# Kernel optimization log

Hardware: AMD Instinct MI355X
Metric: run time of the kernel (lower is better)

## Reference

```python
import jax, jax.numpy as jnp
import numpy as np

B, S, D = 2, 2048, 2048
H, DH = 16, 128  # heads, dhead


def setup_inputs() -> dict:
    key = jax.random.key(0)
    k1, k2, k3 = jax.random.split(key, 3)
    x = jax.random.normal(k1, (B, S, D), dtype=jnp.float32)
    # torch Linear weights: [out_features, in_features], fan_in-scaled init
    w_in = jax.random.normal(k2, (3 * H * DH, D), dtype=jnp.float32) * (1.0 / np.sqrt(D))
    w_out = jax.random.normal(k3, (D, H * DH), dtype=jnp.float32) * (1.0 / np.sqrt(H * DH))
    return {"x": x, "w_in": w_in, "w_out": w_out}


def reference(x, w_in, w_out):
    b, s, _ = x.shape
    # input projection (no bias): [b, s, 3*H*DH]
    projected = jnp.einsum("bsd,ed->bse", x, w_in)
    # view(b, s, H, 3*DH) then chunk along last dim -> q, k, v each [b, s, H, DH]
    projected = projected.reshape(b, s, H, 3 * DH)
    q, k, v = jnp.split(projected, 3, axis=-1)
    # naive path: scores [b, H, s, s]
    scores = jnp.einsum("bqhd,bkhd->bhqk", q, k) * (1.0 / np.sqrt(DH))
    # causal mask (tril keeps, upper triangle -> -inf)
    causal_mask = jnp.tril(jnp.ones((s, s), dtype=bool))
    scores = jnp.where(causal_mask, scores, jnp.float32(-jnp.inf))
    attn = jax.nn.softmax(scores, axis=-1)
    # PV: [b, s, H, DH]
    out = jnp.einsum("bhqk,bkhd->bqhd", attn, v)
    out = out.reshape(b, s, H * DH)
    # output projection (no bias): [b, s, D]
    return jnp.einsum("bse,de->bsd", out, w_out)
```

## Files before the change

kernel.cpp:

```cpp
#include <hip/hip_runtime.h>
#include <hip/hip_bf16.h>
#include <math.h>


typedef short bf16x8 __attribute__((ext_vector_type(8)));
typedef float f32x4 __attribute__((ext_vector_type(4)));

#define NEG_BIG -30000.0f

__device__ __forceinline__ short f2bf(float f) {
    union { float f; unsigned u; } v; v.f = f;
    unsigned r = v.u + 0x7fffu + ((v.u >> 16) & 1u);
    return (short)(r >> 16);
}

__device__ __forceinline__ int pack2bf(float a, float b) {
    return (int)((((unsigned)f2bf(b)) << 16) | (((unsigned)f2bf(a)) & 0xffffu));
}

#define GLDS16(g, l) \
    __builtin_amdgcn_global_load_lds((const __attribute__((address_space(1))) void*)(g), \
                                     (__attribute__((address_space(3))) void*)(l), 16, 0, 0)

__global__ __launch_bounds__(256) void cvt3_f32_bf16(const float* __restrict__ x,  short* __restrict__ dx,
                                                     const float* __restrict__ wi, short* __restrict__ dwi,
                                                     const float* __restrict__ wo, short* __restrict__ dwo,
                                                     int c1, int c2) {
    const int g = blockIdx.x * blockDim.x + threadIdx.x;
    const float* s; short* d; int off;
    if (g < c1)      { s = x;  d = dx;  off = g; }
    else if (g < c2) { s = wi; d = dwi; off = g - c1; }
    else             { s = wo; d = dwo; off = g - c2; }
    float4 v = *(const float4*)(s + (size_t)off * 4);
    short4 o;
    o.x = f2bf(v.x); o.y = f2bf(v.y); o.z = f2bf(v.z); o.w = f2bf(v.w);
    *(short4*)(d + (size_t)off * 4) = o;
}

template <int BN, bool F32OUT>
__global__ __launch_bounds__(256) void gemm_bt(const short* __restrict__ A,
                                               const short* __restrict__ Bm,
                                               void* __restrict__ Cv,
                                               int N, int K) {
    constexpr int NT = BN / 32;
    constexpr int SUBA = 128 * 32;
    constexpr int SUBB = BN * 32;
    __shared__ short sA[2 * SUBA];
    __shared__ short sB[2 * SUBB];
    const int lane = threadIdx.x & 63;
    const int w = threadIdx.x >> 6;
    const int l15 = lane & 15, quad = lane >> 4;
    const int bm0 = blockIdx.y * 128, bn0 = blockIdx.x * BN;

    const int c1 = w * 64 + lane;
    const short* gA = A + (size_t)(bm0 + (c1 >> 2)) * K + (c1 & 3) * 8;
    const short* gB = Bm + (size_t)(bn0 + (c1 >> 2)) * K + (c1 & 3) * 8;
    const size_t half64 = (size_t)64 * K;
    short* lA1 = sA + w * 512;
    short* lA2 = sA + 2048 + w * 512;
    short* lB1 = sB + w * 512;
    short* lB2 = sB + 2048 + w * 512;

    const int wm = (w >> 1) * 64, wn = (w & 1) * (BN / 2);
    const short* pa = sA + (wm + l15) * 32 + quad * 8;
    const short* pb = sB + (wn + l15) * 32 + quad * 8;

    f32x4 acc[4][NT] = {};
    for (int k0 = 0; k0 < K; k0 += 64) {
        #pragma unroll
        for (int s = 0; s < 2; s++) {
            const int ks = k0 + s * 32;
            GLDS16(gA + ks, lA1 + s * SUBA);
            GLDS16(gA + half64 + ks, lA2 + s * SUBA);
            GLDS16(gB + ks, lB1 + s * SUBB);
            if constexpr (BN == 128) GLDS16(gB + half64 + ks, lB2 + s * SUBB);
        }
        __syncthreads();
        #pragma unroll
        for (int s = 0; s < 2; s++) {
            bf16x8 af[4], bf[NT];
            #pragma unroll
            for (int mt = 0; mt < 4; mt++) af[mt] = *(const bf16x8*)(pa + s * SUBA + mt * 512);
            #pragma unroll
            for (int nt = 0; nt < NT; nt++) bf[nt] = *(const bf16x8*)(pb + s * SUBB + nt * 512);
            #pragma unroll
            for (int mt = 0; mt < 4; mt++)
                #pragma unroll
                for (int nt = 0; nt < NT; nt++)
                    acc[mt][nt] = __builtin_amdgcn_mfma_f32_16x16x32_bf16(af[mt], bf[nt], acc[mt][nt], 0, 0, 0);
        }
        __syncthreads();
    }
    #pragma unroll
    for (int mt = 0; mt < 4; mt++)
        #pragma unroll
        for (int nt = 0; nt < NT; nt++)
            #pragma unroll
            for (int r = 0; r < 4; r++) {
                int row = bm0 + wm + mt * 16 + quad * 4 + r;
                int col = bn0 + wn + nt * 16 + l15;
                if (F32OUT)
                    ((float*)Cv)[(size_t)row * N + col] = acc[mt][nt][r];
                else
                    ((short*)Cv)[(size_t)row * N + col] = f2bf(acc[mt][nt][r]);
            }
}

#define VP2 72
__global__ __launch_bounds__(512) void attn_kernel(const short* __restrict__ P,
                                                   short* __restrict__ O) {
    constexpr int S = 2048, ROWW = 6144, HD = 2048;
    const int id = blockIdx.x;
    const int b = id >> 8;
    const int rr = id & 255;
    const int h = rr & 15;
    const int t0 = rr >> 4;
    const int qt = b ? (15 - t0) : t0;
    const int wave = threadIdx.x >> 6, lane = threadIdx.x & 63;
    const int l15 = lane & 15, quad = lane >> 4;
    const int qRow = qt * 128 + wave * 16;
    const short* Pb = P + (size_t)b * S * ROWW;
    const short* Qp = Pb + h * 384;
    const short* Kp = Qp + 128;
    const short* Vp = Qp + 256;

    __shared__ short sK[2][64 * 128];
    __shared__ short sVt[2][128 * VP2];

    bf16x8 qf[4];
    #pragma unroll
    for (int f = 0; f < 4; f++)
        qf[f] = *(const bf16x8*)(Qp + (size_t)(qRow + l15) * ROWW + f * 32 + quad * 8);

    const bool isK = wave < 4;
    const int c1 = (wave & 3) * 64 + lane;
    const int krow1 = c1 >> 4;
    const int kcol = ((c1 & 15) ^ (krow1 & 15)) * 8;
    const short* gK1 = Kp + (size_t)krow1 * ROWW + kcol;
    const short* gK2 = Kp + (size_t)(krow1 + 16) * ROWW + kcol;
    const short* gK3 = Kp + (size_t)(krow1 + 32) * ROWW + kcol;
    const short* gK4 = Kp + (size_t)(krow1 + 48) * ROWW + kcol;
    const int ldsOff1 = (wave & 3) * 512;
    const int ldsOff2 = 2048 + ldsOff1;
    const int ldsOff3 = 4096 + ldsOff1;
    const int ldsOff4 = 6144 + ldsOff1;
    const int vt = (int)threadIdx.x - 256;
    const int vKey = vt & 31;
    const int vD0 = (vt >> 5) * 8;
    const short* gV = Vp + (size_t)vKey * ROWW + vD0;
    const short* gV2 = Vp + (size_t)(vKey + 32) * ROWW + vD0;

    const int kTiles = qt * 2 + 2;
    const float c2 = 0.12752741594977435f;
    const float THRR = 90.50966799f;
    const int qG = qRow + l15;

    f32x4 accO[8] = {};
    float m_i = NEG_BIG, l_i = 0.f;

    if (isK) {
        GLDS16(gK1, &sK[0][ldsOff1]);
        GLDS16(gK2, &sK[0][ldsOff2]);
        GLDS16(gK3, &sK[0][ldsOff3]);
        GLDS16(gK4, &sK[0][ldsOff4]);
    } else {
        bf16x8 v0 = *(const bf16x8*)(gV);
        bf16x8 v1 = *(const bf16x8*)(gV + 64);
        bf16x8 v2 = *(const bf16x8*)(gV2);
        bf16x8 v3 = *(const bf16x8*)(gV2 + 64);
        #pragma unroll
        for (int j = 0; j < 8; j++) {
            sVt[0][(vD0 + j) * VP2 + vKey] = v0[j];
            sVt[0][(vD0 + 64 + j) * VP2 + vKey] = v1[j];
            sVt[0][(vD0 + j) * VP2 + vKey + 32] = v2[j];
            sVt[0][(vD0 + 64 + j) * VP2 + vKey + 32] = v3[j];
        }
    }
    __syncthreads();

    for (int kt = 0; kt < kTiles; kt++) {
        const int cur = kt & 1, nxt = cur ^ 1;
        const bool pre = (kt + 1 < kTiles);
        bf16x8 v0n, v1n, v2n, v3n;
        if (pre) {
            const size_t kOff = (size_t)(kt + 1) * 64 * ROWW;
            if (isK) {
                GLDS16(gK1 + kOff, &sK[nxt][ldsOff1]);
                GLDS16(gK2 + kOff, &sK[nxt][ldsOff2]);
                GLDS16(gK3 + kOff, &sK[nxt][ldsOff3]);
                GLDS16(gK4 + kOff, &sK[nxt][ldsOff4]);
            } else {
                v0n = *(const bf16x8*)(gV + kOff);
                v1n = *(const bf16x8*)(gV + kOff + 64);
                v2n = *(const bf16x8*)(gV2 + kOff);
                v3n = *(const bf16x8*)(gV2 + kOff + 64);
            }
        }
        if (kt * 64 <= qRow + 15) {
            f32x4 sc[4] = {};
            #pragma unroll
            for (int f = 0; f < 4; f++) {
                const int jj = ((4 * f + quad) ^ l15) * 8;
                #pragma unroll
                for (int hh = 0; hh < 4; hh++) {
                    bf16x8 kf = *(const bf16x8*)(&sK[cur][(hh * 16 + l15) * 128 + jj]);
                    sc[hh] = __builtin_amdgcn_mfma_f32_16x16x32_bf16(kf, qf[f], sc[hh], 0, 0, 0);
                }
            }
            if (kt * 64 + 63 > qRow) {
                #pragma unroll
                for (int hh = 0; hh < 4; hh++)
                    #pragma unroll
                    for (int r = 0; r < 4; r++) {
                        const int key = kt * 64 + hh * 16 + quad * 4 + r;
                        if (key > qG) sc[hh][r] = NEG_BIG;
                    }
            }
            float mloc = sc[0][0];
            #pragma unroll
            for (int hh = 0; hh < 4; hh++)
                #pragma unroll
                for (int r = 0; r < 4; r++) mloc = fmaxf(mloc, sc[hh][r]);
            mloc = fmaxf(mloc, __shfl_xor(mloc, 16));
            mloc = fmaxf(mloc, __shfl_xor(mloc, 32));
            if (!__all(mloc <= m_i + THRR)) {
                const float nm = fmaxf(m_i, mloc);
                const float alpha = __builtin_exp2f((m_i - nm) * c2);
                m_i = nm;
                l_i *= alpha;
                #pragma unroll
                for (int t = 0; t < 8; t++)
                    #pragma unroll
                    for (int r = 0; r < 4; r++) accO[t][r] *= alpha;
            }
            const float mc2 = m_i * c2;
            float ssum = 0.f;
            #pragma unroll
            for (int hh = 0; hh < 4; hh++)
                #pragma unroll
                for (int r = 0; r < 4; r++) {
                    float p = __builtin_exp2f(__builtin_fmaf(sc[hh][r], c2, -mc2));
                    sc[hh][r] = p;
                    ssum += p;
                }
            ssum += __shfl_xor(ssum, 16);
            ssum += __shfl_xor(ssum, 32);
            l_i += ssum;
            #pragma unroll
            for (int s = 0; s < 2; s++) {
                const int d00 = pack2bf(sc[2 * s][0], sc[2 * s][1]);
                const int d01 = pack2bf(sc[2 * s][2], sc[2 * s][3]);
                const int d10 = pack2bf(sc[2 * s + 1][0], sc[2 * s + 1][1]);
                const int d11 = pack2bf(sc[2 * s + 1][2], sc[2 * s + 1][3]);
                const int srcA = l15 + ((quad & 1) << 5);
                const int srcB = srcA + 16;
                const int s00 = __shfl(d00, srcA), s01 = __shfl(d01, srcA);
                const int s02 = __shfl(d00, srcB), s03 = __shfl(d01, srcB);
                const int s10 = __shfl(d10, srcA), s11 = __shfl(d11, srcA);
                const int s12 = __shfl(d10, srcB), s13 = __shfl(d11, srcB);
                union { int i[4]; bf16x8 v; } pu;
                const bool lo = quad < 2;
                pu.i[0] = lo ? s00 : s10;
                pu.i[1] = lo ? s01 : s11;
                pu.i[2] = lo ? s02 : s12;
                pu.i[3] = lo ? s03 : s13;
                const bf16x8 pf = pu.v;
                #pragma unroll
                for (int t = 0; t < 8; t++) {
                    bf16x8 vf = *(const bf16x8*)(&sVt[cur][(t * 16 + l15) * VP2 + s * 32 + quad * 8]);
                    accO[t] = __builtin_amdgcn_mfma_f32_16x16x32_bf16(vf, pf, accO[t], 0, 0, 0);
                }
            }
        }
        if (pre && !isK) {
            #pragma unroll
            for (int j = 0; j < 8; j++) {
                sVt[nxt][(vD0 + j) * VP2 + vKey] = v0n[j];
                sVt[nxt][(vD0 + 64 + j) * VP2 + vKey] = v1n[j];
                sVt[nxt][(vD0 + j) * VP2 + vKey + 32] = v2n[j];
                sVt[nxt][(vD0 + 64 + j) * VP2 + vKey + 32] = v3n[j];
            }
        }
        __syncthreads();
    }
    const float inv = 1.0f / l_i;
    #pragma unroll
    for (int t = 0; t < 8; t++) {
        short4 st;
        st.x = f2bf(accO[t][0] * inv);
        st.y = f2bf(accO[t][1] * inv);
        st.z = f2bf(accO[t][2] * inv);
        st.w = f2bf(accO[t][3] * inv);
        *(short4*)(&O[(size_t)(b * S + qG) * HD + h * 128 + t * 16 + quad * 4]) = st;
    }
}

extern "C" void kernel_launch(void* const* d_in, const int* in_sizes, int n_in,
                              void* d_out, int out_size, void* d_ws, size_t ws_size,
                              hipStream_t stream) {
    const float* x     = (const float*)d_in[0];
    const float* w_in  = (const float*)d_in[1];
    const float* w_out = (const float*)d_in[2];
    float* out = (float*)d_out;

    short* Pbuf   = (short*)d_ws;
    short* xObuf  = Pbuf  + (size_t)4096 * 6144;
    short* winb   = xObuf + (size_t)8388608;
    short* woutb  = winb  + (size_t)6144 * 2048;

    dim3 blk(256, 1, 1);
    const int nx = 2 * 2048 * 2048, nwi = 6144 * 2048, nwo = 2048 * 2048;
    const int c1 = nx / 4, c2 = c1 + nwi / 4;
    const int totalBlocks = (nx + nwi + nwo) / 1024;
    hipLaunchKernelGGL(cvt3_f32_bf16, dim3(totalBlocks), blk, 0, stream,
                       x, xObuf, w_in, winb, w_out, woutb, c1, c2);
    hipLaunchKernelGGL((gemm_bt<128, false>), dim3(48, 32, 1), blk, 0, stream,
                       xObuf, winb, (void*)Pbuf, 6144, 2048);
    hipLaunchKernelGGL(attn_kernel, dim3(512, 1, 1), dim3(512, 1, 1), 0, stream, Pbuf, xObuf);
    hipLaunchKernelGGL((gemm_bt<128, true>), dim3(16, 32, 1), blk, 0, stream, xObuf, woutb, (void*)out, 2048, 2048);
}
```

Measured before the change: 374.3 us.

## Triple-buffer K tiles with partial vmcnt waits and XOR-swizzle transposed V in LDS

K tiles now go into a three-slot LDS ring filled by direct global-to-LDS loads two tiles ahead. The end-of-iteration barrier is replaced by a manual s_waitcnt vmcnt(4) so the newest K prefetch can stay in flight across the barrier. The transposed V buffer drops its padded stride of 72 in favour of an XOR swizzle on 8-element chunks, cutting LDS use and aiming to avoid bank conflicts. The hand-written waitcnt relies on exact counts of outstanding loads, which could race if the compiler emits extra vector memory operations.

```diff
diff --git a/kernel.cpp b/kernel.cpp
--- a/kernel.cpp
+++ b/kernel.cpp
@@ -106,7 +106,6 @@
             }
 }
 
-#define VP2 72
 __global__ __launch_bounds__(512) void attn_kernel(const short* __restrict__ P,
                                                    short* __restrict__ O) {
     constexpr int S = 2048, ROWW = 6144, HD = 2048;
@@ -124,8 +123,8 @@
     const short* Kp = Qp + 128;
     const short* Vp = Qp + 256;
 
-    __shared__ short sK[2][64 * 128];
-    __shared__ short sVt[2][128 * VP2];
+    __shared__ short sK[3][64 * 128];
+    __shared__ short sVt[2][128 * 64];
 
     bf16x8 qf[4];
     #pragma unroll
@@ -149,6 +148,7 @@
     const int vD0 = (vt >> 5) * 8;
     const short* gV = Vp + (size_t)vKey * ROWW + vD0;
     const short* gV2 = Vp + (size_t)(vKey + 32) * ROWW + vD0;
+    const int vs0 = vKey >> 3, vb = vKey & 7;
 
     const int kTiles = qt * 2 + 2;
     const float c2 = 0.12752741594977435f;
@@ -163,6 +163,11 @@
         GLDS16(gK2, &sK[0][ldsOff2]);
         GLDS16(gK3, &sK[0][ldsOff3]);
         GLDS16(gK4, &sK[0][ldsOff4]);
+        const size_t o1 = (size_t)64 * ROWW;
+        GLDS16(gK1 + o1, &sK[1][ldsOff1]);
+        GLDS16(gK2 + o1, &sK[1][ldsOff2]);
+        GLDS16(gK3 + o1, &sK[1][ldsOff3]);
+        GLDS16(gK4 + o1, &sK[1][ldsOff4]);
     } else {
         bf16x8 v0 = *(const bf16x8*)(gV);
         bf16x8 v1 = *(const bf16x8*)(gV + 64);
@@ -170,31 +175,35 @@
         bf16x8 v3 = *(const bf16x8*)(gV2 + 64);
         #pragma unroll
         for (int j = 0; j < 8; j++) {
-            sVt[0][(vD0 + j) * VP2 + vKey] = v0[j];
-            sVt[0][(vD0 + 64 + j) * VP2 + vKey] = v1[j];
-            sVt[0][(vD0 + j) * VP2 + vKey + 32] = v2[j];
-            sVt[0][(vD0 + 64 + j) * VP2 + vKey + 32] = v3[j];
+            const int rA = vD0 + j, rB = vD0 + 64 + j;
+            sVt[0][rA * 64 + ((vs0 ^ j) << 3) + vb] = v0[j];
+            sVt[0][rB * 64 + ((vs0 ^ j) << 3) + vb] = v1[j];
+            sVt[0][rA * 64 + (((4 + vs0) ^ j) << 3) + vb] = v2[j];
+            sVt[0][rB * 64 + (((4 + vs0) ^ j) << 3) + vb] = v3[j];
         }
     }
     __syncthreads();
 
+    int c3 = 0;
     for (int kt = 0; kt < kTiles; kt++) {
         const int cur = kt & 1, nxt = cur ^ 1;
         const bool pre = (kt + 1 < kTiles);
         bf16x8 v0n, v1n, v2n, v3n;
-        if (pre) {
+        if (isK) {
+            if (kt + 2 < kTiles) {
+                int s3 = c3 + 2; if (s3 >= 3) s3 -= 3;
+                const size_t kOff = (size_t)(kt + 2) * 64 * ROWW;
+                GLDS16(gK1 + kOff, &sK[s3][ldsOff1]);
+                GLDS16(gK2 + kOff, &sK[s3][ldsOff2]);
+                GLDS16(gK3 + kOff, &sK[s3][ldsOff3]);
+                GLDS16(gK4 + kOff, &sK[s3][ldsOff4]);
+            }
+        } else if (pre) {
             const size_t kOff = (size_t)(kt + 1) * 64 * ROWW;
-            if (isK) {
-                GLDS16(gK1 + kOff, &sK[nxt][ldsOff1]);
-                GLDS16(gK2 + kOff, &sK[nxt][ldsOff2]);
-                GLDS16(gK3 + kOff, &sK[nxt][ldsOff3]);
-                GLDS16(gK4 + kOff, &sK[nxt][ldsOff4]);
-            } else {
-                v0n = *(const bf16x8*)(gV + kOff);
-                v1n = *(const bf16x8*)(gV + kOff + 64);
-                v2n = *(const bf16x8*)(gV2 + kOff);
-                v3n = *(const bf16x8*)(gV2 + kOff + 64);
-            }
+            v0n = *(const bf16x8*)(gV + kOff);
+            v1n = *(const bf16x8*)(gV + kOff + 64);
+            v2n = *(const bf16x8*)(gV2 + kOff);
+            v3n = *(const bf16x8*)(gV2 + kOff + 64);
         }
         if (kt * 64 <= qRow + 15) {
             f32x4 sc[4] = {};
@@ -203,7 +212,7 @@
                 const int jj = ((4 * f + quad) ^ l15) * 8;
                 #pragma unroll
                 for (int hh = 0; hh < 4; hh++) {
-                    bf16x8 kf = *(const bf16x8*)(&sK[cur][(hh * 16 + l15) * 128 + jj]);
+                    bf16x8 kf = *(const bf16x8*)(&sK[c3][(hh * 16 + l15) * 128 + jj]);
                     sc[hh] = __builtin_amdgcn_mfma_f32_16x16x32_bf16(kf, qf[f], sc[hh], 0, 0, 0);
                 }
             }
@@ -267,7 +276,8 @@
                 const bf16x8 pf = pu.v;
                 #pragma unroll
                 for (int t = 0; t < 8; t++) {
-                    bf16x8 vf = *(const bf16x8*)(&sVt[cur][(t * 16 + l15) * VP2 + s * 32 + quad * 8]);
+                    bf16x8 vf = *(const bf16x8*)(
+                        &sVt[cur][(t * 16 + l15) * 64 + (((s * 4 + quad) ^ (l15 & 7)) << 3)]);
                     accO[t] = __builtin_amdgcn_mfma_f32_16x16x32_bf16(vf, pf, accO[t], 0, 0, 0);
                 }
             }
@@ -275,13 +285,20 @@
         if (pre && !isK) {
             #pragma unroll
             for (int j = 0; j < 8; j++) {
-                sVt[nxt][(vD0 + j) * VP2 + vKey] = v0n[j];
-                sVt[nxt][(vD0 + 64 + j) * VP2 + vKey] = v1n[j];
-                sVt[nxt][(vD0 + j) * VP2 + vKey + 32] = v2n[j];
-                sVt[nxt][(vD0 + 64 + j) * VP2 + vKey + 32] = v3n[j];
-            }
-        }
-        __syncthreads();
+                const int rA = vD0 + j, rB = vD0 + 64 + j;
+                sVt[nxt][rA * 64 + ((vs0 ^ j) << 3) + vb] = v0n[j];
+                sVt[nxt][rB * 64 + ((vs0 ^ j) << 3) + vb] = v1n[j];
+                sVt[nxt][rA * 64 + (((4 + vs0) ^ j) << 3) + vb] = v2n[j];
+                sVt[nxt][rB * 64 + (((4 + vs0) ^ j) << 3) + vb] = v3n[j];
+            }
+        }
+        if (isK)
+            asm volatile("s_waitcnt vmcnt(4) lgkmcnt(0)" ::: "memory");
+        else
+            asm volatile("s_waitcnt lgkmcnt(0)" ::: "memory");
+        __builtin_amdgcn_s_barrier();
+        __builtin_amdgcn_sched_barrier(0);
+        c3 = (c3 == 2) ? 0 : c3 + 1;
     }
     const float inv = 1.0f / l_i;
     #pragma unroll
```

New measurement: 379.8 us. About the same (+1.5%).
